# Optimization experiments

Hardware: AMD Instinct MI355X
Metric: run time of the kernel (lower is better)

Reference implementation:

```python
import jax, jax.numpy as jnp
import numpy as np
from jax import lax


def binarize(x):
    # tf.sign with 0 mapped to +1
    return jnp.where(x >= 0, jnp.ones_like(x), -jnp.ones_like(x))


def setup_inputs() -> dict:
    key = jax.random.key(0)
    kx, kw = jax.random.split(key)
    x = jax.random.normal(kx, (64, 56, 56, 128), dtype=jnp.float32)
    # weights init: normal stddev=0.1, shape (kh, kw, in_ch, filters) == HWIO
    w = jax.random.normal(kw, (3, 3, 128, 256), dtype=jnp.float32) * 0.1
    return {"x": x, "w": w}


def reference(x, w):
    x_bin = binarize(x)
    w_bin = binarize(w)
    # NHWC input, HWIO kernel, SAME padding, stride (1,1)
    out = lax.conv_general_dilated(
        x_bin, w_bin,
        window_strides=(1, 1),
        padding="SAME",
        dimension_numbers=("NHWC", "HWIO", "NHWC"),
    )
    return out
```

## Files before the change

### kernel.cpp

```cpp
#include <hip/hip_runtime.h>
#include <stdint.h>


#define IH 56
#define IW 56
#define COUT 256
#define NB 64
#define ROWPX 58
#define PXB 144
#define ROWB (ROWPX * PXB)

typedef int v4i  __attribute__((ext_vector_type(4)));
typedef int v16i __attribute__((ext_vector_type(16)));

__global__ void pack_x_kernel(const float* __restrict__ x,
                              uint64_t* __restrict__ xp, int npix) {
    int gtid = blockIdx.x * blockDim.x + threadIdx.x;
    int wave = gtid >> 6, lane = gtid & 63;
    int nw = (gridDim.x * blockDim.x) >> 6;
    const float2* x2 = (const float2*)x;
    for (int p = wave; p < npix; p += nw) {
        float2 v = x2[(size_t)p * 64 + lane];
        uint64_t m0 = __ballot(v.x < 0.0f);
        uint64_t m1 = __ballot(v.y < 0.0f);
        if (lane == 0) { xp[2 * (size_t)p] = m0; xp[2 * (size_t)p + 1] = m1; }
    }
}

__global__ void pack_w_kernel(const float* __restrict__ w,
                              uint64_t* __restrict__ wp) {
    int gtid = blockIdx.x * blockDim.x + threadIdx.x;
    int wave = gtid >> 6, lane = gtid & 63;
    int nw = (gridDim.x * blockDim.x) >> 6;
    const int ntask = 9 * 2 * COUT;
    for (int t = wave; t < ntask; t += nw) {
        int oc = t & 255, hf = (t >> 8) & 1, tap = t >> 9;
        float v = w[((size_t)(tap * 128 + 2 * lane + hf)) * COUT + oc];
        uint64_t m = __ballot(v < 0.0f);
        if (lane == 0) wp[(size_t)(tap * 2 + hf) * COUT + oc] = m;
    }
}

__global__ void swz_w_kernel(const uint64_t* __restrict__ wp,
                             char* __restrict__ bsw, int* __restrict__ kct) {
    int t = blockIdx.x * blockDim.x + threadIdx.x;
    if (t < 36 * 8 * 64) {
        int lane = t & 63, ntks = t >> 6;
        int nt = ntks & 7, ks = ntks >> 3;
        int oc = nt * 32 + (lane & 31);
        int kk = ks * 32 + (lane >> 5) * 16;
        int tap = kk >> 7, c = kk & 127;
        int hf = c >> 6, bit0 = c & 63;
        uint64_t word = wp[(size_t)(tap * 2 + hf) * COUT + oc];
        int4 d;
        d.x = (int)(((uint32_t)(word >> (bit0 + 0))  & 0xF) * 0x00204081u & 0x01010101u);
        d.y = (int)(((uint32_t)(word >> (bit0 + 4))  & 0xF) * 0x00204081u & 0x01010101u);
        d.z = (int)(((uint32_t)(word >> (bit0 + 8))  & 0xF) * 0x00204081u & 0x01010101u);
        d.w = (int)(((uint32_t)(word >> (bit0 + 12)) & 0xF) * 0x00204081u & 0x01010101u);
        *(int4*)(bsw + (size_t)t * 16) = d;
    } else if (t < 36 * 8 * 64 + 256) {
        int oc = t - 36 * 8 * 64;
        int Sw[9];
#pragma unroll
        for (int tp = 0; tp < 9; ++tp)
            Sw[tp] = __popcll(wp[(size_t)(tp * 2) * COUT + oc]) +
                     __popcll(wp[(size_t)(tp * 2 + 1) * COUT + oc]);
        for (int hc = 0; hc < 3; ++hc)
            for (int wc = 0; wc < 3; ++wc) {
                int K = 0;
                for (int kh = 0; kh < 3; ++kh) {
                    if (hc == 0 && kh == 0) continue;
                    if (hc == 2 && kh == 2) continue;
                    for (int kw = 0; kw < 3; ++kw) {
                        if (wc == 0 && kw == 0) continue;
                        if (wc == 2 && kw == 2) continue;
                        K += 128 - 2 * Sw[kh * 3 + kw];
                    }
                }
                kct[(hc * 3 + wc) * COUT + oc] = K;
            }
    }
}

__global__ __launch_bounds__(256, 2) void bconv_mfma(
        const uint64_t* __restrict__ xp,
        const char* __restrict__ bsw,
        const int* __restrict__ kct,
        float* __restrict__ out) {
    __shared__ alignas(16) char xs8[4 * ROWB];
    __shared__ int pc[4][ROWPX];
    __shared__ int sx9[2][IW];

    int bh = blockIdx.x % 28, n = blockIdx.x / 28;
    int hbase = bh * 2;
    int tid = threadIdx.x;

    for (int t = tid; t < 4 * ROWPX; t += 256) {
        int row = t / ROWPX, col = t % ROWPX;
        int rr = hbase - 1 + row, cc = col - 1;
        uint64_t w0 = 0, w1 = 0;
        if ((unsigned)rr < IH && (unsigned)cc < IW) {
            const uint64_t* pp = xp + 2 * (((size_t)n * IH + rr) * IW + cc);
            w0 = pp[0]; w1 = pp[1];
        }
        pc[row][col] = __popcll(w0) + __popcll(w1);
        uint32_t* dst = (uint32_t*)(xs8 + row * ROWB + col * PXB);
#pragma unroll
        for (int i = 0; i < 16; ++i)
            dst[i] = ((uint32_t)(w0 >> (4 * i)) & 0xF) * 0x00204081u & 0x01010101u;
#pragma unroll
        for (int i = 0; i < 16; ++i)
            dst[16 + i] = ((uint32_t)(w1 >> (4 * i)) & 0xF) * 0x00204081u & 0x01010101u;
    }
    __syncthreads();

    for (int t = tid; t < 2 * IW; t += 256) {
        int g = t / IW, px = t % IW;
        int s = 0;
#pragma unroll
        for (int kh = 0; kh < 3; ++kh)
            s += pc[g + kh][px] + pc[g + kh][px + 1] + pc[g + kh][px + 2];
        sx9[g][px] = s;
    }
    __syncthreads();

    int wv = tid >> 6, lane = tid & 63;
    int g = wv >> 1;
    int nt0 = (wv & 1) * 4;
    int m = lane & 31, half = lane >> 5;

    v16i acc[2][4];
#pragma unroll
    for (int mt = 0; mt < 2; ++mt)
#pragma unroll
        for (int j = 0; j < 4; ++j)
#pragma unroll
            for (int r = 0; r < 16; ++r) acc[mt][j][r] = 0;

    const v4i* bbase = (const v4i*)bsw + (size_t)nt0 * 64 + lane;

    for (int tap = 0; tap < 9; ++tap) {
        int kh = tap / 3, kw = tap % 3;
        const char* arow = xs8 + (g + kh) * ROWB + kw * PXB;
#pragma unroll
        for (int kc = 0; kc < 4; ++kc) {
            int choff = kc * 32 + half * 16;
            v4i a0 = *(const v4i*)(arow + (0  + m) * PXB + choff);
            v4i a1 = *(const v4i*)(arow + (24 + m) * PXB + choff);
            int ks = tap * 4 + kc;
            const v4i* bp = bbase + (size_t)ks * 8 * 64;
#pragma unroll
            for (int j = 0; j < 4; ++j) {
                v4i b = bp[j * 64];
                acc[0][j] = __builtin_amdgcn_mfma_i32_32x32x32_i8(a0, b, acc[0][j], 0, 0, 0);
                acc[1][j] = __builtin_amdgcn_mfma_i32_32x32x32_i8(a1, b, acc[1][j], 0, 0, 0);
            }
        }
    }

    int h = hbase + g;
    int hc = (h == 0) ? 0 : ((h == IH - 1) ? 2 : 1);
    float* orow = out + (((size_t)n * IH + h) * IW) * COUT;

    int sxv[2][16];
#pragma unroll
    for (int r = 0; r < 16; ++r) {
        int pxr = (r & 3) + 8 * (r >> 2) + 4 * half;
        sxv[0][r] = sx9[g][pxr];
        sxv[1][r] = sx9[g][24 + pxr];
    }

#pragma unroll
    for (int j = 0; j < 4; ++j) {
        int ocj = (nt0 + j) * 32 + m;
        int Ki  = kct[(hc * 3 + 1) * COUT + ocj];
        int K0  = kct[(hc * 3 + 0) * COUT + ocj];
        int K55 = kct[(hc * 3 + 2) * COUT + ocj];
#pragma unroll
        for (int mt = 0; mt < 2; ++mt) {
            int Mb = mt ? 24 : 0;
#pragma unroll
            for (int r = 0; r < 16; ++r) {
                int pxr = (r & 3) + 8 * (r >> 2) + 4 * half;
                int px = Mb + pxr;
                int K = Ki;
                if (mt == 0 && r == 0 && half == 0) K = K0;
                if (mt == 1 && r == 15 && half == 1) K = K55;
                float o = (float)(K - 2 * sxv[mt][r] + 4 * acc[mt][j][r]);
                orow[(size_t)px * COUT + ocj] = o;
            }
        }
    }
}

extern "C" void kernel_launch(void* const* d_in, const int* in_sizes, int n_in,
                              void* d_out, int out_size, void* d_ws, size_t ws_size,
                              hipStream_t stream) {
    const float* x = (const float*)d_in[0];
    const float* w = (const float*)d_in[1];
    float* out = (float*)d_out;

    uint64_t* wp  = (uint64_t*)d_ws;
    int*      kct = (int*)((char*)d_ws + 36864);
    char*     bsw = (char*)d_ws + 46080;
    uint64_t* xp  = (uint64_t*)((char*)d_ws + 344064);

    const int npix = NB * IH * IW;

    pack_x_kernel<<<6272, 256, 0, stream>>>(x, xp, npix);
    pack_w_kernel<<<288, 256, 0, stream>>>(w, wp);
    swz_w_kernel<<<73, 256, 0, stream>>>(wp, bsw, kct);
    bconv_mfma<<<NB * 28, 256, 0, stream>>>(xp, bsw, kct, out);
}
```

Before: 370.6 us.

## Software-pipeline B fragment loads, vectorize LDS staging, batch pack_x per wave

The main MFMA loop now prefetches the weight (B) fragments from global memory two k-steps ahead using a triple register buffer, so global load latency overlaps the MFMA work. The LDS staging of unpacked input bits switches from 32 scalar stores to 8 int4 stores per pixel. pack_x_kernel now has each wave handle four pixels per iteration, giving more loads in flight. These changes raise register pressure under the 256-thread, 2-block launch bound, and the wrap-around prefetch at the end loads redundant data.

```diff
diff --git a/kernel.cpp b/kernel.cpp
--- a/kernel.cpp
+++ b/kernel.cpp
@@ -13,17 +13,32 @@
 typedef int v4i  __attribute__((ext_vector_type(4)));
 typedef int v16i __attribute__((ext_vector_type(16)));
 
+__device__ __forceinline__ uint32_t nib(uint64_t w, int i) {
+    return ((uint32_t)(w >> (4 * i)) & 0xF) * 0x00204081u & 0x01010101u;
+}
+
 __global__ void pack_x_kernel(const float* __restrict__ x,
                               uint64_t* __restrict__ xp, int npix) {
     int gtid = blockIdx.x * blockDim.x + threadIdx.x;
     int wave = gtid >> 6, lane = gtid & 63;
     int nw = (gridDim.x * blockDim.x) >> 6;
     const float2* x2 = (const float2*)x;
-    for (int p = wave; p < npix; p += nw) {
-        float2 v = x2[(size_t)p * 64 + lane];
-        uint64_t m0 = __ballot(v.x < 0.0f);
-        uint64_t m1 = __ballot(v.y < 0.0f);
-        if (lane == 0) { xp[2 * (size_t)p] = m0; xp[2 * (size_t)p + 1] = m1; }
+    int q = npix >> 2;
+    for (int p = wave; p < q; p += nw) {
+        float2 v0 = x2[(size_t)p * 64 + lane];
+        float2 v1 = x2[((size_t)p + q) * 64 + lane];
+        float2 v2 = x2[((size_t)p + 2 * q) * 64 + lane];
+        float2 v3 = x2[((size_t)p + 3 * q) * 64 + lane];
+        uint64_t a0 = __ballot(v0.x < 0.0f), a1 = __ballot(v0.y < 0.0f);
+        uint64_t b0 = __ballot(v1.x < 0.0f), b1 = __ballot(v1.y < 0.0f);
+        uint64_t c0 = __ballot(v2.x < 0.0f), c1 = __ballot(v2.y < 0.0f);
+        uint64_t d0 = __ballot(v3.x < 0.0f), d1 = __ballot(v3.y < 0.0f);
+        if (lane == 0) {
+            xp[2 * (size_t)p] = a0;             xp[2 * (size_t)p + 1] = a1;
+            xp[2 * ((size_t)p + q)] = b0;       xp[2 * ((size_t)p + q) + 1] = b1;
+            xp[2 * ((size_t)p + 2 * q)] = c0;   xp[2 * ((size_t)p + 2 * q) + 1] = c1;
+            xp[2 * ((size_t)p + 3 * q)] = d0;   xp[2 * ((size_t)p + 3 * q) + 1] = d1;
+        }
     }
 }
 
@@ -53,10 +68,10 @@
         int hf = c >> 6, bit0 = c & 63;
         uint64_t word = wp[(size_t)(tap * 2 + hf) * COUT + oc];
         int4 d;
-        d.x = (int)(((uint32_t)(word >> (bit0 + 0))  & 0xF) * 0x00204081u & 0x01010101u);
-        d.y = (int)(((uint32_t)(word >> (bit0 + 4))  & 0xF) * 0x00204081u & 0x01010101u);
-        d.z = (int)(((uint32_t)(word >> (bit0 + 8))  & 0xF) * 0x00204081u & 0x01010101u);
-        d.w = (int)(((uint32_t)(word >> (bit0 + 12)) & 0xF) * 0x00204081u & 0x01010101u);
+        d.x = (int)nib(word, (bit0 >> 2) + 0);
+        d.y = (int)nib(word, (bit0 >> 2) + 1);
+        d.z = (int)nib(word, (bit0 >> 2) + 2);
+        d.w = (int)nib(word, (bit0 >> 2) + 3);
         *(int4*)(bsw + (size_t)t * 16) = d;
     } else if (t < 36 * 8 * 64 + 256) {
         int oc = t - 36 * 8 * 64;
@@ -104,13 +119,25 @@
             w0 = pp[0]; w1 = pp[1];
         }
         pc[row][col] = __popcll(w0) + __popcll(w1);
-        uint32_t* dst = (uint32_t*)(xs8 + row * ROWB + col * PXB);
-#pragma unroll
-        for (int i = 0; i < 16; ++i)
-            dst[i] = ((uint32_t)(w0 >> (4 * i)) & 0xF) * 0x00204081u & 0x01010101u;
-#pragma unroll
-        for (int i = 0; i < 16; ++i)
-            dst[16 + i] = ((uint32_t)(w1 >> (4 * i)) & 0xF) * 0x00204081u & 0x01010101u;
+        int4* dst4 = (int4*)(xs8 + row * ROWB + col * PXB);
+#pragma unroll
+        for (int gi = 0; gi < 4; ++gi) {
+            int4 d;
+            d.x = (int)nib(w0, 4 * gi + 0);
+            d.y = (int)nib(w0, 4 * gi + 1);
+            d.z = (int)nib(w0, 4 * gi + 2);
+            d.w = (int)nib(w0, 4 * gi + 3);
+            dst4[gi] = d;
+        }
+#pragma unroll
+        for (int gi = 0; gi < 4; ++gi) {
+            int4 d;
+            d.x = (int)nib(w1, 4 * gi + 0);
+            d.y = (int)nib(w1, 4 * gi + 1);
+            d.z = (int)nib(w1, 4 * gi + 2);
+            d.w = (int)nib(w1, 4 * gi + 3);
+            dst4[4 + gi] = d;
+        }
     }
     __syncthreads();
 
@@ -138,24 +165,42 @@
             for (int r = 0; r < 16; ++r) acc[mt][j][r] = 0;
 
     const v4i* bbase = (const v4i*)bsw + (size_t)nt0 * 64 + lane;
-
-    for (int tap = 0; tap < 9; ++tap) {
-        int kh = tap / 3, kw = tap % 3;
-        const char* arow = xs8 + (g + kh) * ROWB + kw * PXB;
-#pragma unroll
-        for (int kc = 0; kc < 4; ++kc) {
-            int choff = kc * 32 + half * 16;
-            v4i a0 = *(const v4i*)(arow + (0  + m) * PXB + choff);
-            v4i a1 = *(const v4i*)(arow + (24 + m) * PXB + choff);
-            int ks = tap * 4 + kc;
-            const v4i* bp = bbase + (size_t)ks * 8 * 64;
-#pragma unroll
-            for (int j = 0; j < 4; ++j) {
-                v4i b = bp[j * 64];
-                acc[0][j] = __builtin_amdgcn_mfma_i32_32x32x32_i8(a0, b, acc[0][j], 0, 0, 0);
-                acc[1][j] = __builtin_amdgcn_mfma_i32_32x32x32_i8(a1, b, acc[1][j], 0, 0, 0);
-            }
-        }
+    const char* abase = xs8 + g * ROWB + half * 16 + m * PXB;
+
+    v4i b0[4], b1[4], b2[4];
+
+#define LB(buf, ks)                                              \
+    do {                                                         \
+        const v4i* _p = bbase + (size_t)(ks) * 512;              \
+        buf[0] = _p[0];   buf[1] = _p[64];                       \
+        buf[2] = _p[128]; buf[3] = _p[192];                      \
+    } while (0)
+
+#define STEPK(ks, buf)                                           \
+    do {                                                         \
+        int _tap = (ks) >> 2, _kc = (ks) & 3;                    \
+        const char* _ar = abase + (_tap / 3) * ROWB +            \
+                          (_tap % 3) * PXB + _kc * 32;           \
+        v4i _a0 = *(const v4i*)(_ar);                            \
+        v4i _a1 = *(const v4i*)(_ar + 24 * PXB);                 \
+        _Pragma("unroll")                                        \
+        for (int _j = 0; _j < 4; ++_j) {                         \
+            acc[0][_j] = __builtin_amdgcn_mfma_i32_32x32x32_i8(  \
+                _a0, buf[_j], acc[0][_j], 0, 0, 0);              \
+            acc[1][_j] = __builtin_amdgcn_mfma_i32_32x32x32_i8(  \
+                _a1, buf[_j], acc[1][_j], 0, 0, 0);              \
+        }                                                        \
+    } while (0)
+
+    LB(b0, 0);
+    LB(b1, 1);
+    for (int ks = 0; ks < 36; ks += 3) {
+        LB(b2, ks + 2);
+        STEPK(ks, b0);
+        LB(b0, (ks + 3 < 36) ? ks + 3 : 0);
+        STEPK(ks + 1, b1);
+        LB(b1, (ks + 4 < 36) ? ks + 4 : 0);
+        STEPK(ks + 2, b2);
     }
 
     int h = hbase + g;
```

Measured after the change: 364.4 us. Within noise of the previous version (-1.7%).
